# Performance work log

Measured on AMD Instinct MI355X. Metric: run time of the kernel, lower is better.

Reference implementation:

```python
import jax, jax.numpy as jnp
import numpy as np
import math

D_MODEL = 768
B, S = 8, 2048


def setup_inputs() -> dict:
    key = jax.random.key(0)
    k1, k2, k3, k4, k5 = jax.random.split(key, 5)
    return {
        "input": jax.random.normal(k1, (B, S, D_MODEL), dtype=jnp.float32),
        "attention_mask": jax.random.randint(k2, (B,), 0, S + 1, dtype=jnp.int32),
        "Wq": jax.random.normal(k3, (D_MODEL, D_MODEL), dtype=jnp.float32),
        "Wk": jax.random.normal(k4, (D_MODEL, D_MODEL), dtype=jnp.float32),
        "Wv": jax.random.normal(k5, (D_MODEL, D_MODEL), dtype=jnp.float32),
    }


def reference(input, attention_mask, Wq, Wk, Wv):
    d_model = Wq.shape[0]
    # QKV projections (v is computed in the original but never used in the output)
    q = jnp.matmul(input, Wq)  # [B,S,D]
    k = jnp.matmul(input, Wk)  # [B,S,D]
    v = jnp.matmul(input, Wv)  # [B,S,D] (dead in original forward output)
    # Per-sample QK^T, vectorized instead of the original python loop+cat
    attention_score = jnp.einsum("bqd,bkd->bqk", q, k) / math.sqrt(float(d_model) ** 3)
    # Ragged mask: positions (j,k) with j<len_i and k<len_i keep the score, else -1000.
    # Built with vectorized arange comparisons instead of the original triple python loop.
    idx = jnp.arange(attention_score.shape[1])  # [S]
    valid = idx[None, :] < attention_mask[:, None]  # [B,S]
    keep = valid[:, :, None] & valid[:, None, :]  # [B,S,S]
    mask_attention_score = jnp.where(keep, attention_score, jnp.float32(-1000.0))
    attention_score_n = jax.nn.softmax(mask_attention_score, axis=-1)  # computed but unused, as in original
    # Original returns UNMASKED, pre-softmax scores matmul'd with the raw input (not v).
    self_attention = jnp.einsum("bqk,bkd->bqd", attention_score, input)
    return self_attention
```

## Files before the change

### kernel.cpp

```cpp
#include <hip/hip_runtime.h>
#include <cmath>


typedef __attribute__((ext_vector_type(8))) short short8;
typedef __attribute__((ext_vector_type(4))) float f32x4;

__device__ __forceinline__ unsigned short f2bf(float f) {
    union { float f; unsigned int u; } v; v.f = f;
    unsigned int u = v.u;
    return (unsigned short)((u + 0x7FFFu + ((u >> 16) & 1u)) >> 16);
}

template <int ROWS>
__device__ __forceinline__ void stage_glds(const unsigned short* src, unsigned short* lds,
                                           int ld, int tid)
{
    #pragma unroll
    for (int it = 0; it < ROWS / 32; ++it) {
        int slot = it * 256 + tid;
        int r = slot >> 3, c = slot & 7;
        const unsigned short* gp = src + (size_t)r * ld + ((c ^ (r & 7)) << 3);
        unsigned short* lp = lds + (size_t)(it * 256 + (tid & 192)) * 8;
        __builtin_amdgcn_global_load_lds(
            (__attribute__((address_space(1))) void*)(void*)gp,
            (__attribute__((address_space(3))) void*)lp, 16, 0, 0);
    }
}

template <int ROWS>
__device__ __forceinline__ void stage_f32(const float* __restrict__ src, unsigned short* lds,
                                          int ld, int tid)
{
    #pragma unroll
    for (int it = 0; it < ROWS / 32; ++it) {
        int slot = it * 256 + tid;
        int r = slot >> 3, c = slot & 7;
        const float* gp = src + (size_t)r * ld + c * 8;
        float4 a = *reinterpret_cast<const float4*>(gp);
        float4 d = *reinterpret_cast<const float4*>(gp + 4);
        union { short8 s; unsigned short u[8]; } v;
        v.u[0] = f2bf(a.x); v.u[1] = f2bf(a.y); v.u[2] = f2bf(a.z); v.u[3] = f2bf(a.w);
        v.u[4] = f2bf(d.x); v.u[5] = f2bf(d.y); v.u[6] = f2bf(d.z); v.u[7] = f2bf(d.w);
        *reinterpret_cast<short8*>(&lds[r * 64 + ((c ^ (r & 7)) << 3)]) = v.s;
    }
}

template <int ROWS>
__device__ __forceinline__ void stage_f32pair(const float* __restrict__ a,
                                              const float* __restrict__ b,
                                              unsigned short* lds, int ld, int tid)
{
    #pragma unroll
    for (int it = 0; it < ROWS / 32; ++it) {
        int slot = it * 256 + tid;
        int r = slot >> 3, c = slot & 7;
        size_t off = (size_t)r * ld + c * 8;
        float4 a0 = *reinterpret_cast<const float4*>(a + off);
        float4 a1 = *reinterpret_cast<const float4*>(a + off + 4);
        float4 b0 = *reinterpret_cast<const float4*>(b + off);
        float4 b1 = *reinterpret_cast<const float4*>(b + off + 4);
        union { short8 s; unsigned short u[8]; } v;
        v.u[0] = f2bf(a0.x + b0.x); v.u[1] = f2bf(a0.y + b0.y);
        v.u[2] = f2bf(a0.z + b0.z); v.u[3] = f2bf(a0.w + b0.w);
        v.u[4] = f2bf(a1.x + b1.x); v.u[5] = f2bf(a1.y + b1.y);
        v.u[6] = f2bf(a1.z + b1.z); v.u[7] = f2bf(a1.w + b1.w);
        *reinterpret_cast<short8*>(&lds[r * 64 + ((c ^ (r & 7)) << 3)]) = v.s;
    }
}

template <int TM, int TN>
__device__ __forceinline__ void mfma_step(const unsigned short* __restrict__ Al,
                                          const unsigned short* __restrict__ Bl,
                                          f32x4 (&acc)[TM / 32][TN / 32],
                                          int wr, int wc, int l15, int quad)
{
    constexpr int FM = TM / 32, FN = TN / 32;
    short8 af[FM][2], bfr[FN][2];
    #pragma unroll
    for (int i = 0; i < FM; ++i) {
        int ra = wr + i * 16 + l15;
        af[i][0] = *reinterpret_cast<const short8*>(&Al[ra * 64 + ((quad ^ (ra & 7)) << 3)]);
        af[i][1] = *reinterpret_cast<const short8*>(&Al[ra * 64 + (((quad + 4) ^ (ra & 7)) << 3)]);
    }
    #pragma unroll
    for (int i = 0; i < FN; ++i) {
        int rb = wc + i * 16 + l15;
        bfr[i][0] = *reinterpret_cast<const short8*>(&Bl[rb * 64 + ((quad ^ (rb & 7)) << 3)]);
        bfr[i][1] = *reinterpret_cast<const short8*>(&Bl[rb * 64 + (((quad + 4) ^ (rb & 7)) << 3)]);
    }
    #pragma unroll
    for (int ks = 0; ks < 2; ++ks)
        #pragma unroll
        for (int mi = 0; mi < FM; ++mi)
            #pragma unroll
            for (int ni = 0; ni < FN; ++ni)
                acc[mi][ni] = __builtin_amdgcn_mfma_f32_16x16x32_bf16(
                    af[mi][ks], bfr[ni][ks], acc[mi][ni], 0, 0, 0);
}

__device__ __forceinline__ void store_c(float* C, size_t i, float v) { C[i] = v; }
__device__ __forceinline__ void store_c(unsigned short* C, size_t i, float v) { C[i] = f2bf(v); }

template <int TM, int TN, typename CT>
__device__ __forceinline__ void epilogue(CT* __restrict__ C, f32x4 (&acc)[TM / 32][TN / 32],
                                         int rowBase, int colBase, int ldc, float alpha,
                                         int wr, int wc, int l15, int quad)
{
    #pragma unroll
    for (int mi = 0; mi < TM / 32; ++mi)
        #pragma unroll
        for (int ni = 0; ni < TN / 32; ++ni) {
            int col = colBase + wc + ni * 16 + l15;
            #pragma unroll
            for (int r = 0; r < 4; ++r) {
                int row = rowBase + wr + mi * 16 + quad * 4 + r;
                store_c(C, (size_t)row * ldc + col, alpha * acc[mi][ni][r]);
            }
        }
}

__device__ void transp_tile(const float* __restrict__ X, unsigned short* __restrict__ Xt,
                            unsigned short* __restrict__ Xbf, int bb, int s0, int d0,
                            unsigned short* tbuf )
{
    const float* Xb = X + (size_t)bb * 2048 * 768;
    unsigned short* Xtb = Xt + (size_t)bb * 2048 * 768;
    unsigned short* Xbb = Xbf + (size_t)bb * 2048 * 768;
    const int tx = threadIdx.x & 7, ty = threadIdx.x >> 3;

    float4 v = *reinterpret_cast<const float4*>(&Xb[(size_t)(s0 + ty) * 768 + d0 + tx * 4]);
    ushort4 pk;
    pk.x = f2bf(v.x); pk.y = f2bf(v.y); pk.z = f2bf(v.z); pk.w = f2bf(v.w);
    *reinterpret_cast<ushort4*>(&Xbb[(size_t)(s0 + ty) * 768 + d0 + tx * 4]) = pk;
    tbuf[(tx * 4 + 0) * 36 + ty] = pk.x;
    tbuf[(tx * 4 + 1) * 36 + ty] = pk.y;
    tbuf[(tx * 4 + 2) * 36 + ty] = pk.z;
    tbuf[(tx * 4 + 3) * 36 + ty] = pk.w;
    __syncthreads();
    ushort4 o;
    o.x = tbuf[ty * 36 + tx * 4 + 0];
    o.y = tbuf[ty * 36 + tx * 4 + 1];
    o.z = tbuf[ty * 36 + tx * 4 + 2];
    o.w = tbuf[ty * 36 + tx * 4 + 3];
    *reinterpret_cast<ushort4*>(&Xtb[(size_t)(d0 + ty) * 2048 + s0 + tx * 4]) = o;
}

__global__ __launch_bounds__(256)
void prep(const float* __restrict__ X, const float* __restrict__ Wq,
          const float* __restrict__ Wk, unsigned short* __restrict__ Xt,
          unsigned short* __restrict__ Xbf, unsigned short* __restrict__ P16)
{
    __shared__ unsigned short lds[(64 + 64) * 64];
    const int blk = blockIdx.x;
    const int tid = threadIdx.x, lane = tid & 63, wave = tid >> 6;
    const int l15 = lane & 15, quad = lane >> 4;

    if (blk < 144) {
        const int ty = blk / 12, tz = blk - ty * 12;
        const int wr = (wave >> 1) * 32, wc = (wave & 1) * 32;
        f32x4 acc[2][2] = {};
        for (int k0 = 0; k0 < 768; k0 += 64) {
            stage_f32<64>(Wq + (size_t)ty * 64 * 768 + k0, lds, 768, tid);
            stage_f32<64>(Wk + (size_t)tz * 64 * 768 + k0, lds + 64 * 64, 768, tid);
            __syncthreads();
            mfma_step<64, 64>(lds, lds + 64 * 64, acc, wr, wc, l15, quad);
            __syncthreads();
        }
        epilogue<64, 64, unsigned short>(P16, acc, ty * 64, tz * 64, 768, 1.0f,
                                         wr, wc, l15, quad);
    } else {
        const int t0 = blk - 144;
        const int b = t0 / 1536, t = t0 - b * 1536;
        transp_tile(X, Xt, Xbf, b, (t & 63) * 32, (t >> 6) * 32, lds);
    }
}

__global__ __launch_bounds__(256)
void gemm_G(const unsigned short* __restrict__ Xt, float* __restrict__ Ga,
            float* __restrict__ Gb)
{
    __shared__ unsigned short lds[(96 + 96) * 64];
    const int b = blockIdx.x, ty = blockIdx.y;
    const int tz = blockIdx.z >> 1, ks = blockIdx.z & 1;
    const int tid = threadIdx.x, lane = tid & 63, wave = tid >> 6;
    const int wr = (wave >> 1) * 48, wc = (wave & 1) * 48;
    const int l15 = lane & 15, quad = lane >> 4;

    const unsigned short* Xtb = Xt + (size_t)b * 768 * 2048;
    const unsigned short* A0 = Xtb + (size_t)ty * 96 * 2048 + ks * 1024;
    const unsigned short* B0 = Xtb + (size_t)tz * 96 * 2048 + ks * 1024;
    float* C = (ks ? Gb : Ga) + (size_t)b * 768 * 768;

    f32x4 acc[3][3] = {};
    for (int k0 = 0; k0 < 1024; k0 += 64) {
        stage_glds<96>(A0 + k0, lds, 2048, tid);
        stage_glds<96>(B0 + k0, lds + 96 * 64, 2048, tid);
        __syncthreads();
        mfma_step<96, 96>(lds, lds + 96 * 64, acc, wr, wc, l15, quad);
        __syncthreads();
    }
    epilogue<96, 96, float>(C, acc, ty * 96, tz * 96, 768, 1.0f, wr, wc, l15, quad);
}

__global__ __launch_bounds__(256)
void gemm_Ht(const float* __restrict__ Ga, const float* __restrict__ Gb,
             const unsigned short* __restrict__ P16, unsigned short* __restrict__ Ht,
             float alpha)
{
    __shared__ unsigned short lds[(64 + 64) * 64];
    const int b = blockIdx.x, ty = blockIdx.y, tz = blockIdx.z;
    const int tid = threadIdx.x, lane = tid & 63, wave = tid >> 6;
    const int wr = (wave >> 1) * 32, wc = (wave & 1) * 32;
    const int l15 = lane & 15, quad = lane >> 4;

    const float* Ab = Ga + (size_t)b * 768 * 768 + (size_t)ty * 64 * 768;
    const float* Bb = Gb + (size_t)b * 768 * 768 + (size_t)ty * 64 * 768;
    const unsigned short* B0 = P16 + (size_t)tz * 64 * 768;

    f32x4 acc[2][2] = {};
    for (int k0 = 0; k0 < 768; k0 += 64) {
        stage_f32pair<64>(Ab + k0, Bb + k0, lds, 768, tid);
        stage_glds<64>(B0 + k0, lds + 64 * 64, 768, tid);
        __syncthreads();
        mfma_step<64, 64>(lds, lds + 64 * 64, acc, wr, wc, l15, quad);
        __syncthreads();
    }
    epilogue<64, 64, unsigned short>(Ht + (size_t)b * 768 * 768, acc,
                                     ty * 64, tz * 64, 768, alpha, wr, wc, l15, quad);
}

__global__ __launch_bounds__(256)
void gemm_out(const unsigned short* __restrict__ Xbf, const unsigned short* __restrict__ Ht,
              float* __restrict__ out)
{
    __shared__ unsigned short lds[(128 + 64) * 64];
    const int b = blockIdx.x, ty = blockIdx.y, tz = blockIdx.z;
    const int tid = threadIdx.x, lane = tid & 63, wave = tid >> 6;
    const int wr = (wave >> 1) * 64, wc = (wave & 1) * 32;
    const int l15 = lane & 15, quad = lane >> 4;

    const unsigned short* A0 = Xbf + (size_t)b * 2048 * 768 + (size_t)ty * 128 * 768;
    const unsigned short* B0 = Ht + (size_t)b * 768 * 768 + (size_t)tz * 64 * 768;

    f32x4 acc[4][2] = {};
    for (int k0 = 0; k0 < 768; k0 += 64) {
        stage_glds<128>(A0 + k0, lds, 768, tid);
        stage_glds<64>(B0 + k0, lds + 128 * 64, 768, tid);
        __syncthreads();
        mfma_step<128, 64>(lds, lds + 128 * 64, acc, wr, wc, l15, quad);
        __syncthreads();
    }
    epilogue<128, 64, float>(out + (size_t)b * 2048 * 768, acc,
                             ty * 128, tz * 64, 768, 1.0f, wr, wc, l15, quad);
}

extern "C" void kernel_launch(void* const* d_in, const int* in_sizes, int n_in,
                              void* d_out, int out_size, void* d_ws, size_t ws_size,
                              hipStream_t stream)
{
    const float* X  = (const float*)d_in[0];
    const float* Wq = (const float*)d_in[2];
    const float* Wk = (const float*)d_in[3];
    float* out = (float*)d_out;

    const int Bn = 8, S = 2048, D = 768;
    const float alpha = 1.0f / (768.0f * sqrtf(768.0f));
    const size_t szX  = (size_t)Bn * S * D;
    const size_t szDD = (size_t)Bn * D * D;

    unsigned short* Xt  = (unsigned short*)d_ws;
    unsigned short* Xbf = Xt + szX;
    unsigned short* P16 = Xbf + szX;
    float* Ga = (float*)(P16 + (size_t)D * D);
    float* Gb = Ga + szDD;
    unsigned short* Ht = (unsigned short*)(Gb + szDD);

    prep<<<dim3(144 + Bn * (S / 32) * (D / 32)), 256, 0, stream>>>(X, Wq, Wk, Xt, Xbf, P16);

    gemm_G<<<dim3(Bn, 8, 16), 256, 0, stream>>>(Xt, Ga, Gb);

    gemm_Ht<<<dim3(Bn, 12, 12), 256, 0, stream>>>(Ga, Gb, P16, Ht, alpha);

    gemm_out<<<dim3(Bn, S / 128, 12), 256, 0, stream>>>(Xbf, Ht, out);
}
```

Before: 199.8 us.

## Move Wq·Wk product into Gram GEMM launch and widen transpose tiles

The small Wq×Wk^T product (P16) moves out of the prep kernel and into the same launch as the X^T X Gram GEMM, as extra tail blocks. Prep becomes a pure cast-and-transpose kernel using 64x64 tiles, with each thread handling a 4x4 sub-block, an XOR-swizzled LDS buffer and 16-byte stores. The intent is to make the transpose bandwidth-efficient and to overlap the weight GEMM with the Gram GEMM rather than the memory-bound transpose. The Gram-kernel block order is also changed, putting batch in the low bits.

```diff
diff --git a/kernel.cpp b/kernel.cpp
--- a/kernel.cpp
+++ b/kernel.cpp
@@ -119,44 +119,96 @@
         }
 }
 
-__device__ void transp_tile(const float* __restrict__ X, unsigned short* __restrict__ Xt,
-                            unsigned short* __restrict__ Xbf, int bb, int s0, int d0,
-                            unsigned short* tbuf )
-{
-    const float* Xb = X + (size_t)bb * 2048 * 768;
-    unsigned short* Xtb = Xt + (size_t)bb * 2048 * 768;
-    unsigned short* Xbb = Xbf + (size_t)bb * 2048 * 768;
-    const int tx = threadIdx.x & 7, ty = threadIdx.x >> 3;
-
-    float4 v = *reinterpret_cast<const float4*>(&Xb[(size_t)(s0 + ty) * 768 + d0 + tx * 4]);
-    ushort4 pk;
-    pk.x = f2bf(v.x); pk.y = f2bf(v.y); pk.z = f2bf(v.z); pk.w = f2bf(v.w);
-    *reinterpret_cast<ushort4*>(&Xbb[(size_t)(s0 + ty) * 768 + d0 + tx * 4]) = pk;
-    tbuf[(tx * 4 + 0) * 36 + ty] = pk.x;
-    tbuf[(tx * 4 + 1) * 36 + ty] = pk.y;
-    tbuf[(tx * 4 + 2) * 36 + ty] = pk.z;
-    tbuf[(tx * 4 + 3) * 36 + ty] = pk.w;
+__global__ __launch_bounds__(256)
+void prep(const float* __restrict__ X, unsigned short* __restrict__ Xt,
+          unsigned short* __restrict__ Xbf)
+{
+    __shared__ unsigned short T[64 * 64];
+    const int blk = blockIdx.x;
+    const int b = blk & 7;
+    const int tile = blk >> 3;
+    const int s0 = (tile & 31) * 64;
+    const int d0 = (tile >> 5) * 64;
+    const float* Xb = X + (size_t)b * 2048 * 768;
+    unsigned short* Xtb = Xt + (size_t)b * 2048 * 768;
+    unsigned short* Xbb = Xbf + (size_t)b * 2048 * 768;
+
+    const int mr = threadIdx.x >> 4;
+    const int mc = threadIdx.x & 15;
+
+    const float* src = &Xb[(size_t)(s0 + 4 * mr) * 768 + d0 + 4 * mc];
+    float4 v0 = *reinterpret_cast<const float4*>(src);
+    float4 v1 = *reinterpret_cast<const float4*>(src + 768);
+    float4 v2 = *reinterpret_cast<const float4*>(src + 2 * 768);
+    float4 v3 = *reinterpret_cast<const float4*>(src + 3 * 768);
+    ushort4 r0 = { f2bf(v0.x), f2bf(v0.y), f2bf(v0.z), f2bf(v0.w) };
+    ushort4 r1 = { f2bf(v1.x), f2bf(v1.y), f2bf(v1.z), f2bf(v1.w) };
+    ushort4 r2 = { f2bf(v2.x), f2bf(v2.y), f2bf(v2.z), f2bf(v2.w) };
+    ushort4 r3 = { f2bf(v3.x), f2bf(v3.y), f2bf(v3.z), f2bf(v3.w) };
+    unsigned short* dstb = &Xbb[(size_t)(s0 + 4 * mr) * 768 + d0 + 4 * mc];
+    *reinterpret_cast<ushort4*>(dstb)            = r0;
+    *reinterpret_cast<ushort4*>(dstb + 768)      = r1;
+    *reinterpret_cast<ushort4*>(dstb + 2 * 768)  = r2;
+    *reinterpret_cast<ushort4*>(dstb + 3 * 768)  = r3;
+
+    ushort4 c0 = { r0.x, r1.x, r2.x, r3.x };
+    ushort4 c1 = { r0.y, r1.y, r2.y, r3.y };
+    ushort4 c2 = { r0.z, r1.z, r2.z, r3.z };
+    ushort4 c3 = { r0.w, r1.w, r2.w, r3.w };
+
+    {
+        int d;
+        d = 4 * mc + 0; *reinterpret_cast<ushort4*>(&T[d * 64 + ((mr ^ (2 * (d & 7))) & 15) * 4]) = c0;
+        d = 4 * mc + 1; *reinterpret_cast<ushort4*>(&T[d * 64 + ((mr ^ (2 * (d & 7))) & 15) * 4]) = c1;
+        d = 4 * mc + 2; *reinterpret_cast<ushort4*>(&T[d * 64 + ((mr ^ (2 * (d & 7))) & 15) * 4]) = c2;
+        d = 4 * mc + 3; *reinterpret_cast<ushort4*>(&T[d * 64 + ((mr ^ (2 * (d & 7))) & 15) * 4]) = c3;
+    }
     __syncthreads();
-    ushort4 o;
-    o.x = tbuf[ty * 36 + tx * 4 + 0];
-    o.y = tbuf[ty * 36 + tx * 4 + 1];
-    o.z = tbuf[ty * 36 + tx * 4 + 2];
-    o.w = tbuf[ty * 36 + tx * 4 + 3];
-    *reinterpret_cast<ushort4*>(&Xtb[(size_t)(d0 + ty) * 2048 + s0 + tx * 4]) = o;
+
+    #pragma unroll
+    for (int p = 0; p < 2; ++p) {
+        int d  = p * 32 + (threadIdx.x >> 3);
+        int q0 = 2 * (threadIdx.x & 7);
+        int c  = (q0 ^ (2 * (d & 7))) & 15;
+        short8 o = *reinterpret_cast<const short8*>(&T[d * 64 + c * 4]);
+        *reinterpret_cast<short8*>(&Xtb[(size_t)(d0 + d) * 2048 + s0 + q0 * 4]) = o;
+    }
 }
 
 __global__ __launch_bounds__(256)
-void prep(const float* __restrict__ X, const float* __restrict__ Wq,
-          const float* __restrict__ Wk, unsigned short* __restrict__ Xt,
-          unsigned short* __restrict__ Xbf, unsigned short* __restrict__ P16)
-{
-    __shared__ unsigned short lds[(64 + 64) * 64];
+void gemm_GP(const unsigned short* __restrict__ Xt, float* __restrict__ Ga,
+             float* __restrict__ Gb, const float* __restrict__ Wq,
+             const float* __restrict__ Wk, unsigned short* __restrict__ P16)
+{
+    __shared__ unsigned short lds[(96 + 96) * 64];
     const int blk = blockIdx.x;
     const int tid = threadIdx.x, lane = tid & 63, wave = tid >> 6;
     const int l15 = lane & 15, quad = lane >> 4;
 
-    if (blk < 144) {
-        const int ty = blk / 12, tz = blk - ty * 12;
+    if (blk < 1024) {
+        const int b = blk & 7;
+        const int ty = (blk >> 3) & 7;
+        const int zz = blk >> 6;
+        const int tz = zz >> 1, ks = zz & 1;
+        const int wr = (wave >> 1) * 48, wc = (wave & 1) * 48;
+
+        const unsigned short* Xtb = Xt + (size_t)b * 768 * 2048;
+        const unsigned short* A0 = Xtb + (size_t)ty * 96 * 2048 + ks * 1024;
+        const unsigned short* B0 = Xtb + (size_t)tz * 96 * 2048 + ks * 1024;
+        float* C = (ks ? Gb : Ga) + (size_t)b * 768 * 768;
+
+        f32x4 acc[3][3] = {};
+        for (int k0 = 0; k0 < 1024; k0 += 64) {
+            stage_glds<96>(A0 + k0, lds, 2048, tid);
+            stage_glds<96>(B0 + k0, lds + 96 * 64, 2048, tid);
+            __syncthreads();
+            mfma_step<96, 96>(lds, lds + 96 * 64, acc, wr, wc, l15, quad);
+            __syncthreads();
+        }
+        epilogue<96, 96, float>(C, acc, ty * 96, tz * 96, 768, 1.0f, wr, wc, l15, quad);
+    } else {
+        const int pb = blk - 1024;
+        const int ty = pb / 12, tz = pb - ty * 12;
         const int wr = (wave >> 1) * 32, wc = (wave & 1) * 32;
         f32x4 acc[2][2] = {};
         for (int k0 = 0; k0 < 768; k0 += 64) {
@@ -168,38 +220,7 @@
         }
         epilogue<64, 64, unsigned short>(P16, acc, ty * 64, tz * 64, 768, 1.0f,
                                          wr, wc, l15, quad);
-    } else {
-        const int t0 = blk - 144;
-        const int b = t0 / 1536, t = t0 - b * 1536;
-        transp_tile(X, Xt, Xbf, b, (t & 63) * 32, (t >> 6) * 32, lds);
-    }
-}
-
-__global__ __launch_bounds__(256)
-void gemm_G(const unsigned short* __restrict__ Xt, float* __restrict__ Ga,
-            float* __restrict__ Gb)
-{
-    __shared__ unsigned short lds[(96 + 96) * 64];
-    const int b = blockIdx.x, ty = blockIdx.y;
-    const int tz = blockIdx.z >> 1, ks = blockIdx.z & 1;
-    const int tid = threadIdx.x, lane = tid & 63, wave = tid >> 6;
-    const int wr = (wave >> 1) * 48, wc = (wave & 1) * 48;
-    const int l15 = lane & 15, quad = lane >> 4;
-
-    const unsigned short* Xtb = Xt + (size_t)b * 768 * 2048;
-    const unsigned short* A0 = Xtb + (size_t)ty * 96 * 2048 + ks * 1024;
-    const unsigned short* B0 = Xtb + (size_t)tz * 96 * 2048 + ks * 1024;
-    float* C = (ks ? Gb : Ga) + (size_t)b * 768 * 768;
-
-    f32x4 acc[3][3] = {};
-    for (int k0 = 0; k0 < 1024; k0 += 64) {
-        stage_glds<96>(A0 + k0, lds, 2048, tid);
-        stage_glds<96>(B0 + k0, lds + 96 * 64, 2048, tid);
-        __syncthreads();
-        mfma_step<96, 96>(lds, lds + 96 * 64, acc, wr, wc, l15, quad);
-        __syncthreads();
-    }
-    epilogue<96, 96, float>(C, acc, ty * 96, tz * 96, 768, 1.0f, wr, wc, l15, quad);
+    }
 }
 
 __global__ __launch_bounds__(256)
@@ -275,9 +296,9 @@
     float* Gb = Ga + szDD;
     unsigned short* Ht = (unsigned short*)(Gb + szDD);
 
-    prep<<<dim3(144 + Bn * (S / 32) * (D / 32)), 256, 0, stream>>>(X, Wq, Wk, Xt, Xbf, P16);
-
-    gemm_G<<<dim3(Bn, 8, 16), 256, 0, stream>>>(Xt, Ga, Gb);
+    prep<<<dim3(Bn * (S / 64) * (D / 64)), 256, 0, stream>>>(X, Xt, Xbf);
+
+    gemm_GP<<<dim3(1024 + 144), 256, 0, stream>>>(Xt, Ga, Gb, Wq, Wk, P16);
 
     gemm_Ht<<<dim3(Bn, 12, 12), 256, 0, stream>>>(Ga, Gb, P16, Ht, alpha);
 
```

Measured after the change: 203.4 us. No clear change (+1.8%).
